# Kernel optimization log

Measured on AMD Instinct MI355X. Metric: run time of the kernel, lower is better.

The kernel has to match this reference:

```python
import jax, jax.numpy as jnp
import numpy as np

BN_EPS = 1e-5

def conv1x1(x, w, b):
    # x: (b, c, t, h, w); w: (o, c); b: (o,)
    return jnp.einsum('bcthw,oc->bothw', x, w) + b[None, :, None, None, None]

def pool_1x2x2(x):
    # MaxPool3d(kernel=(1,2,2), stride=(1,2,2))
    b, c, t, h, w = x.shape
    return x.reshape(b, c, t, h // 2, 2, w // 2, 2).max(axis=(4, 6))

def setup_inputs() -> dict:
    key = jax.random.key(0)
    ks = jax.random.split(key, 12)
    B, C, CI, T, H, W = 2, 256, 128, 16, 28, 28
    s_in = 1.0 / np.sqrt(C)
    s_ci = 1.0 / np.sqrt(CI)
    return {
        'x': jax.random.normal(ks[0], (B, C, T, H, W), jnp.float32),
        'mask_pred': jax.random.normal(ks[1], (B, C, T, H, W), jnp.float32),
        'g_w': jax.random.normal(ks[2], (CI, C), jnp.float32) * s_in,
        'g_b': jax.random.normal(ks[3], (CI,), jnp.float32) * s_in,
        'theta_w': jax.random.normal(ks[4], (CI, C), jnp.float32) * s_in,
        'theta_b': jax.random.normal(ks[5], (CI,), jnp.float32) * s_in,
        'phi_w': jax.random.normal(ks[6], (CI, C), jnp.float32) * s_in,
        'phi_b': jax.random.normal(ks[7], (CI,), jnp.float32) * s_in,
        'W_w': jax.random.normal(ks[8], (C, CI), jnp.float32) * s_ci,
        'W_b': jax.random.normal(ks[9], (C,), jnp.float32) * s_ci,
        'bn_gamma': jax.random.normal(ks[10], (C,), jnp.float32) * 0.1 + 1.0,
        'bn_beta': jax.random.normal(ks[11], (C,), jnp.float32) * 0.1,
    }

def reference(x, mask_pred, g_w, g_b, theta_w, theta_b, phi_w, phi_b, W_w, W_b, bn_gamma, bn_beta):
    B, C, T, H, W = x.shape
    CI = g_w.shape[0]
    # g and phi: 1x1 conv then (1,2,2) max-pool (sub_sample=True)
    g_x = pool_1x2x2(conv1x1(x, g_w, g_b)).reshape(B, CI, -1)          # (b, ci, Ns)
    g_x = g_x.transpose(0, 2, 1)                                        # (b, Ns, ci)
    theta = conv1x1(mask_pred, theta_w, theta_b).reshape(B, CI, -1)     # (b, ci, N)
    theta = theta.transpose(0, 2, 1)                                    # (b, N, ci)
    phi = pool_1x2x2(conv1x1(x, phi_w, phi_b)).reshape(B, CI, -1)       # (b, ci, Ns)
    f = jnp.einsum('bnc,bcm->bnm', theta, phi)                          # (b, N, Ns)
    f_div_C = jax.nn.softmax(f, axis=1)                                 # softmax over N (dim=1)
    y = jnp.einsum('bnm,bmc->bnc', f_div_C, g_x)                        # (b, N, ci)
    y = y.transpose(0, 2, 1).reshape(B, CI, T, H, W)
    W_y = conv1x1(y, W_w, W_b)                                          # (b, c, t, h, w)
    # BatchNorm3d in training mode (batch statistics over b,t,h,w)
    mean = W_y.mean(axis=(0, 2, 3, 4), keepdims=True)
    var = W_y.var(axis=(0, 2, 3, 4), keepdims=True)
    W_y = (W_y - mean) * jax.lax.rsqrt(var + BN_EPS)
    W_y = W_y * bn_gamma[None, :, None, None, None] + bn_beta[None, :, None, None, None]
    return W_y + x
```

## Files before the change

### kernel.cpp

```cpp
#include <hip/hip_runtime.h>


#define B_ 2
#define C_ 256
#define CI_ 128
#define NPIX 12544
#define NS 3136
#define NSL 28

typedef short bf16x8 __attribute__((ext_vector_type(8)));
typedef float f32x4 __attribute__((ext_vector_type(4)));

__device__ __forceinline__ short f2bf(float f) {
    unsigned u = __float_as_uint(f);
    u = (u + 0x7fff + ((u >> 16) & 1)) >> 16;
    return (short)u;
}
__device__ __forceinline__ float bf2f(short s) {
    return __uint_as_float(((unsigned)(unsigned short)s) << 16);
}
__device__ __forceinline__ short f2h(float f) {
    _Float16 h = (_Float16)f;
    short s;
    __builtin_memcpy(&s, &h, 2);
    return s;
}
__device__ __forceinline__ float h2f(short s) {
    _Float16 h;
    __builtin_memcpy(&h, &s, 2);
    return (float)h;
}
__device__ __forceinline__ f32x4 mfma16(bf16x8 a, bf16x8 b, f32x4 c) {
    return __builtin_amdgcn_mfma_f32_16x16x32_bf16(a, b, c, 0, 0, 0);
}
__device__ __forceinline__ size_t pidx(int r, int k) {
    return (size_t)((r >> 4) * 4 + (k >> 5)) * 512 +
           (size_t)(((k >> 3) & 3) * 128 + (r & 15) * 8 + (k & 7));
}
__device__ __forceinline__ size_t pidx256(int r, int k) {
    return (size_t)((r >> 4) * 8 + (k >> 5)) * 512 +
           (size_t)(((k >> 3) & 3) * 128 + (r & 15) * 8 + (k & 7));
}

struct Frag3 { bf16x8 h, m, l; };
struct Frag2 { bf16x8 h, m; };

__device__ __forceinline__ Frag3 ld3(const short* __restrict__ h, const short* __restrict__ m,
                                     const short* __restrict__ l, size_t off) {
    Frag3 f;
    f.h = *(const bf16x8*)(h + off);
    f.m = *(const bf16x8*)(m + off);
    f.l = *(const bf16x8*)(l + off);
    return f;
}
__device__ __forceinline__ Frag2 ld2(const short* __restrict__ h, const short* __restrict__ m,
                                     size_t off) {
    Frag2 f;
    f.h = *(const bf16x8*)(h + off);
    f.m = *(const bf16x8*)(m + off);
    return f;
}
__device__ __forceinline__ f32x4 mm5(Frag2 a, Frag3 w, f32x4 acc) {
    acc = mfma16(a.h, w.l, acc);
    acc = mfma16(a.m, w.m, acc);
    acc = mfma16(a.m, w.h, acc);
    acc = mfma16(a.h, w.m, acc);
    acc = mfma16(a.h, w.h, acc);
    return acc;
}
__device__ __forceinline__ f32x4 mm3(Frag2 a, Frag2 b, f32x4 acc) {
    acc = mfma16(a.m, b.h, acc);
    acc = mfma16(a.h, b.m, acc);
    acc = mfma16(a.h, b.h, acc);
    return acc;
}
__device__ __forceinline__ f32x4 mm2s(bf16x8 ah, Frag2 b, f32x4 acc) {
    acc = mfma16(ah, b.m, acc);
    acc = mfma16(ah, b.h, acc);
    return acc;
}
__device__ __forceinline__ bf16x8 mk_pa(f32x4 f0, f32x4 f1, int srcLo, int srcHi, bool hiTile) {
    unsigned t0d0 = (unsigned)(unsigned short)f2bf(__expf(f0[0] - 32.f)) |
                    ((unsigned)(unsigned short)f2bf(__expf(f0[1] - 32.f)) << 16);
    unsigned t0d1 = (unsigned)(unsigned short)f2bf(__expf(f0[2] - 32.f)) |
                    ((unsigned)(unsigned short)f2bf(__expf(f0[3] - 32.f)) << 16);
    unsigned t1d0 = (unsigned)(unsigned short)f2bf(__expf(f1[0] - 32.f)) |
                    ((unsigned)(unsigned short)f2bf(__expf(f1[1] - 32.f)) << 16);
    unsigned t1d1 = (unsigned)(unsigned short)f2bf(__expf(f1[2] - 32.f)) |
                    ((unsigned)(unsigned short)f2bf(__expf(f1[3] - 32.f)) << 16);
    unsigned lo0t0 = __shfl(t0d0, srcLo), lo1t0 = __shfl(t0d1, srcLo);
    unsigned hi0t0 = __shfl(t0d0, srcHi), hi1t0 = __shfl(t0d1, srcHi);
    unsigned lo0t1 = __shfl(t1d0, srcLo), lo1t1 = __shfl(t1d1, srcLo);
    unsigned hi0t1 = __shfl(t1d0, srcHi), hi1t1 = __shfl(t1d1, srcHi);
    unsigned pd[4];
    pd[0] = hiTile ? lo0t1 : lo0t0;
    pd[1] = hiTile ? lo1t1 : lo1t0;
    pd[2] = hiTile ? hi0t1 : hi0t0;
    pd[3] = hiTile ? hi1t1 : hi1t0;
    bf16x8 pa;
    __builtin_memcpy(&pa, pd, 16);
    return pa;
}

__global__ void k_splitw(const float* __restrict__ thw, const float* __restrict__ phw,
                         const float* __restrict__ gw, const float* __restrict__ Ww,
                         short* __restrict__ thwH, short* __restrict__ thwM, short* __restrict__ thwL,
                         short* __restrict__ phwH, short* __restrict__ phwM, short* __restrict__ phwL,
                         short* __restrict__ gwH, short* __restrict__ gwM,
                         short* __restrict__ wwH, short* __restrict__ wwM) {
    int i = blockIdx.x * 256 + threadIdx.x;
    int which = i >> 15, j = i & 32767;
    if (which == 0) {
        float x = thw[j];
        unsigned uh = __float_as_uint(x) & 0xffff0000u;
        float r1 = x - __uint_as_float(uh);
        unsigned um = __float_as_uint(r1) & 0xffff0000u;
        thwH[j] = (short)(uh >> 16);
        thwM[j] = (short)(um >> 16);
        thwL[j] = f2bf(r1 - __uint_as_float(um));
    } else if (which == 1) {
        float x = phw[j];
        unsigned uh = __float_as_uint(x) & 0xffff0000u;
        float r1 = x - __uint_as_float(uh);
        unsigned um = __float_as_uint(r1) & 0xffff0000u;
        phwH[j] = (short)(uh >> 16);
        phwM[j] = (short)(um >> 16);
        phwL[j] = f2bf(r1 - __uint_as_float(um));
    } else if (which == 2) {
        float x = gw[j];
        unsigned uh = __float_as_uint(x) & 0xffff0000u;
        gwH[j] = (short)(uh >> 16);
        gwM[j] = f2bf(x - __uint_as_float(uh));
    } else {
        float x = Ww[j];
        unsigned uh = __float_as_uint(x) & 0xffff0000u;
        wwH[j] = (short)(uh >> 16);
        wwM[j] = f2bf(x - __uint_as_float(uh));
    }
}

__global__ void k_transpose2p(const float* __restrict__ src, short* __restrict__ oh,
                              short* __restrict__ om) {
    __shared__ float tile[32][33];
    int b = blockIdx.z;
    const float* s = src + (size_t)b * C_ * NPIX;
    size_t ob = (size_t)b * NPIX * C_;
    int p0 = blockIdx.x * 32, c0 = blockIdx.y * 32;
    for (int i = threadIdx.y; i < 32; i += 8)
        tile[i][threadIdx.x] = s[(size_t)(c0 + i) * NPIX + p0 + threadIdx.x];
    __syncthreads();
    for (int i = threadIdx.y; i < 32; i += 8) {
        float v = tile[threadIdx.x][i];
        unsigned uh = __float_as_uint(v) & 0xffff0000u;
        size_t o = ob + pidx256(p0 + i, c0 + threadIdx.x);
        oh[o] = (short)(uh >> 16);
        om[o] = f2bf(v - __uint_as_float(uh));
    }
}

__global__ __launch_bounds__(128, 2) void k_conv5(const short* __restrict__ AH,
        const short* __restrict__ AM,
        const short* __restrict__ WH, const short* __restrict__ WM, const short* __restrict__ WL,
        const float* __restrict__ bias, short* __restrict__ oh, short* __restrict__ om) {
    int wid = threadIdx.x >> 6, lane = threadIdx.x & 63;
    int quad = lane >> 4, l16 = lane & 15;
    int b = blockIdx.y;
    size_t ab = (size_t)b * NPIX * C_;
    size_t ob = (size_t)b * NPIX * CI_;
    int rt0 = blockIdx.x * 2;
    f32x4 acc[2][4] = {};
    for (int kt = 0; kt < 8; kt++) {
        Frag2 a0 = ld2(AH, AM, ab + ((size_t)rt0 * 8 + kt) * 512 + lane * 8);
        Frag2 a1 = ld2(AH, AM, ab + ((size_t)(rt0 + 1) * 8 + kt) * 512 + lane * 8);
#pragma unroll
        for (int c4 = 0; c4 < 4; c4++) {
            int c = (wid * 4 + c4) * 16 + l16;
            Frag3 w = ld3(WH, WM, WL, (size_t)c * C_ + kt * 32 + quad * 8);
            acc[0][c4] = mm5(a0, w, acc[0][c4]);
            acc[1][c4] = mm5(a1, w, acc[1][c4]);
        }
    }
#pragma unroll
    for (int t2 = 0; t2 < 2; t2++)
#pragma unroll
        for (int c4 = 0; c4 < 4; c4++) {
            int c = (wid * 4 + c4) * 16 + l16;
            float bv = bias[c];
#pragma unroll
            for (int r = 0; r < 4; r++) {
                float v = acc[t2][c4][r] + bv;
                unsigned uh = __float_as_uint(v) & 0xffff0000u;
                size_t o = ob + pidx((rt0 + t2) * 16 + quad * 4 + r, c);
                oh[o] = (short)(uh >> 16);
                om[o] = f2bf(v - __uint_as_float(uh));
            }
        }
}

__global__ __launch_bounds__(128, 2) void k_convxg5(const short* __restrict__ AH,
        const short* __restrict__ AM,
        const short* __restrict__ PH, const short* __restrict__ PM, const short* __restrict__ PL,
        const short* __restrict__ GH, const short* __restrict__ GM,
        const float* __restrict__ pbias, const float* __restrict__ gbias,
        float* __restrict__ pfull, short* __restrict__ gout) {
    int wid = threadIdx.x >> 6, lane = threadIdx.x & 63;
    int quad = lane >> 4, l16 = lane & 15;
    int b = blockIdx.y;
    size_t ab = (size_t)b * NPIX * C_;
    float* Pb = pfull + (size_t)b * NPIX * CI_;
    short* Gb = gout + (size_t)b * NPIX * CI_;
    int rt0 = blockIdx.x * 2;
    f32x4 accp[2][4] = {}, accg[2][4] = {};
    for (int kt = 0; kt < 8; kt++) {
        Frag2 a0 = ld2(AH, AM, ab + ((size_t)rt0 * 8 + kt) * 512 + lane * 8);
        Frag2 a1 = ld2(AH, AM, ab + ((size_t)(rt0 + 1) * 8 + kt) * 512 + lane * 8);
#pragma unroll
        for (int c4 = 0; c4 < 4; c4++) {
            int c = (wid * 4 + c4) * 16 + l16;
            size_t wo = (size_t)c * C_ + kt * 32 + quad * 8;
            Frag3 wp = ld3(PH, PM, PL, wo);
            accp[0][c4] = mm5(a0, wp, accp[0][c4]);
            accp[1][c4] = mm5(a1, wp, accp[1][c4]);
            Frag2 wg = ld2(GH, GM, wo);
            accg[0][c4] = mm3(a0, wg, accg[0][c4]);
            accg[1][c4] = mm3(a1, wg, accg[1][c4]);
        }
    }
#pragma unroll
    for (int t2 = 0; t2 < 2; t2++)
#pragma unroll
        for (int c4 = 0; c4 < 4; c4++) {
            int c = (wid * 4 + c4) * 16 + l16;
            float pbv = pbias[c], gbv = gbias[c];
#pragma unroll
            for (int r = 0; r < 4; r++) {
                size_t o = (size_t)((rt0 + t2) * 16 + quad * 4 + r) * CI_ + c;
                Pb[o] = accp[t2][c4][r] + pbv;
                Gb[o] = f2bf(accg[t2][c4][r] + gbv);
            }
        }
}

__global__ void k_pool(const float* __restrict__ pfull, const short* __restrict__ gfull,
                       short* __restrict__ pth, short* __restrict__ ptm,
                       float* __restrict__ gcf) {
    int b = blockIdx.y;
    int idx = blockIdx.x * 256 + threadIdx.x;
    int ci = idx & 127, m = idx >> 7;
    int t = m / 196, r2i = m - t * 196;
    int h2 = r2i / 14, w2 = r2i - h2 * 14;
    size_t p = (size_t)t * 784 + (size_t)(2 * h2) * 28 + 2 * w2;
    size_t i0 = (size_t)b * NPIX * CI_ + p * CI_ + ci;
    float pv = fmaxf(fmaxf(pfull[i0], pfull[i0 + CI_]),
                     fmaxf(pfull[i0 + 28 * CI_], pfull[i0 + 29 * CI_]));
    unsigned uh = __float_as_uint(pv) & 0xffff0000u;
    size_t ob = (size_t)b * NS * CI_ + pidx(m, ci);
    pth[ob] = (short)(uh >> 16);
    ptm[ob] = f2bf(pv - __uint_as_float(uh));
    float g0 = fmaxf(fmaxf(bf2f(gfull[i0]), bf2f(gfull[i0 + CI_])),
                     fmaxf(bf2f(gfull[i0 + 28 * CI_]), bf2f(gfull[i0 + 29 * CI_])));
    gcf[(size_t)b * NS * CI_ + (size_t)ci * NS + m] = g0;
}

__global__ __launch_bounds__(128, 2) void k_stats(
        const short* __restrict__ thh, const short* __restrict__ thm,
        const short* __restrict__ phh, const short* __restrict__ phm,
        float* __restrict__ Spart) {
    (void)thm;
    int wid = threadIdx.x >> 6, lane = threadIdx.x & 63;
    int quad = lane >> 4, l16 = lane & 15;
    int wg = blockIdx.x;
    int p = wg % 56;
    int bx = wg / 56;
    int b = p & 1, ychunk = p >> 1;
    size_t tb = (size_t)b * NPIX * CI_, pb = (size_t)b * NS * CI_;
    int mtA = bx * 4 + wid * 2;
    Frag2 bfA[4], bfB[4];
#pragma unroll
    for (int kk = 0; kk < 4; kk++) {
        bfA[kk] = ld2(phh, phm, pb + ((size_t)mtA * 4 + kk) * 512 + lane * 8);
        bfB[kk] = ld2(phh, phm, pb + ((size_t)(mtA + 1) * 4 + kk) * 512 + lane * 8);
    }
    float SA = 0.f, SB = 0.f;
    int t_beg = ychunk * (784 / NSL), t_end = t_beg + 784 / NSL;
    for (int t = t_beg; t < t_end; t += 2) {
        f32x4 aA0 = {}, aA1 = {}, aB0 = {}, aB1 = {};
#pragma unroll
        for (int kk = 0; kk < 4; kk++) {
            bf16x8 x0 = *(const bf16x8*)(thh + tb + ((size_t)t * 4 + kk) * 512 + lane * 8);
            bf16x8 x1 = *(const bf16x8*)(thh + tb + ((size_t)(t + 1) * 4 + kk) * 512 + lane * 8);
            aA0 = mm2s(x0, bfA[kk], aA0);
            aA1 = mm2s(x1, bfA[kk], aA1);
            aB0 = mm2s(x0, bfB[kk], aB0);
            aB1 = mm2s(x1, bfB[kk], aB1);
        }
        SA += __expf(aA0[0] - 32.f) + __expf(aA0[1] - 32.f) +
              __expf(aA0[2] - 32.f) + __expf(aA0[3] - 32.f) +
              __expf(aA1[0] - 32.f) + __expf(aA1[1] - 32.f) +
              __expf(aA1[2] - 32.f) + __expf(aA1[3] - 32.f);
        SB += __expf(aB0[0] - 32.f) + __expf(aB0[1] - 32.f) +
              __expf(aB0[2] - 32.f) + __expf(aB0[3] - 32.f) +
              __expf(aB1[0] - 32.f) + __expf(aB1[1] - 32.f) +
              __expf(aB1[2] - 32.f) + __expf(aB1[3] - 32.f);
    }
    SA += __shfl_xor(SA, 16, 64); SA += __shfl_xor(SA, 32, 64);
    SB += __shfl_xor(SB, 16, 64); SB += __shfl_xor(SB, 32, 64);
    if (quad == 0) {
        size_t o = ((size_t)(b * NSL + ychunk)) * NS;
        Spart[o + mtA * 16 + l16] = SA;
        Spart[o + (mtA + 1) * 16 + l16] = SB;
    }
}

__global__ void k_combine(const float* __restrict__ Spart, float* __restrict__ wS) {
    int i = blockIdx.x * 256 + threadIdx.x;
    if (i >= B_ * NS) return;
    int b = i / NS, m = i - b * NS;
    float s = 0.f;
#pragma unroll
    for (int sl = 0; sl < NSL; sl++)
        s += Spart[((size_t)(b * NSL + sl)) * NS + m];
    wS[i] = 1.f / s;
}

__global__ void k_gscale(const float* __restrict__ gcf, const float* __restrict__ wS,
                         short* __restrict__ gc) {
    int i = blockIdx.x * 256 + threadIdx.x;
    int b = i / (CI_ * (NS / 8));
    int rem = i - b * CI_ * (NS / 8);
    int c = rem / (NS / 8);
    int m8 = rem - c * (NS / 8);
    int m = m8 * 8;
    const float* gr = gcf + ((size_t)b * CI_ + c) * NS + m;
    const float* wr = wS + (size_t)b * NS + m;
    short* go = gc + (size_t)b * NS * CI_ + ((size_t)(m8 >> 2) * 8 + (c >> 4)) * 512 +
                (m8 & 3) * 128 + (c & 15) * 8;
#pragma unroll
    for (int j = 0; j < 8; j++) go[j] = f2bf(gr[j] * wr[j]);
}

__global__ __launch_bounds__(128, 2) void k_pv(
        const short* __restrict__ thh, const short* __restrict__ thm,
        const short* __restrict__ phh, const short* __restrict__ phm,
        const short* __restrict__ gp, short* __restrict__ part) {
    int wid = threadIdx.x >> 6, lane = threadIdx.x & 63;
    int quad = lane >> 4, l16 = lane & 15;
    int wg = blockIdx.x;
    int pair = wg & 7;
    int bx = wg >> 3;
    int slice = pair >> 1, b = pair & 1;
    int ntA = bx * 4 + wid * 2;
    size_t tb = (size_t)b * NPIX * CI_, pb = (size_t)b * NS * CI_;
    const short* gpb = gp + (size_t)b * NS * CI_;
    Frag2 afA[4], afB[4];
#pragma unroll
    for (int kk = 0; kk < 4; kk++) {
        afA[kk] = ld2(thh, thm, tb + ((size_t)ntA * 4 + kk) * 512 + lane * 8);
        afB[kk] = ld2(thh, thm, tb + ((size_t)(ntA + 1) * 4 + kk) * 512 + lane * 8);
    }
    f32x4 yaccA[8] = {}, yaccB[8] = {};
    int srcLo = ((2 * quad) & 3) * 16 + l16;
    int srcHi = ((2 * quad + 1) & 3) * 16 + l16;
    bool hiTile = quad >= 2;
    int s_beg = slice * 24 + (slice < 2 ? slice : 2);
    int s_end = s_beg + 24 + (slice < 2 ? 1 : 0);
    for (int s = s_beg; s < s_end; s++) {
        bf16x8 gf0 = *(const bf16x8*)(gpb + (size_t)s * 4096 + 0 * 512 + lane * 8);
        bf16x8 gf1 = *(const bf16x8*)(gpb + (size_t)s * 4096 + 1 * 512 + lane * 8);
        bf16x8 gf2 = *(const bf16x8*)(gpb + (size_t)s * 4096 + 2 * 512 + lane * 8);
        bf16x8 gf3 = *(const bf16x8*)(gpb + (size_t)s * 4096 + 3 * 512 + lane * 8);
        bf16x8 gf4 = *(const bf16x8*)(gpb + (size_t)s * 4096 + 4 * 512 + lane * 8);
        bf16x8 gf5 = *(const bf16x8*)(gpb + (size_t)s * 4096 + 5 * 512 + lane * 8);
        bf16x8 gf6 = *(const bf16x8*)(gpb + (size_t)s * 4096 + 6 * 512 + lane * 8);
        bf16x8 gf7 = *(const bf16x8*)(gpb + (size_t)s * 4096 + 7 * 512 + lane * 8);
        f32x4 fA0 = {}, fA1 = {}, fB0 = {}, fB1 = {};
#pragma unroll
        for (int kk = 0; kk < 4; kk++) {
            Frag2 p0 = ld2(phh, phm, pb + ((size_t)(2 * s) * 4 + kk) * 512 + lane * 8);
            Frag2 p1 = ld2(phh, phm, pb + ((size_t)(2 * s + 1) * 4 + kk) * 512 + lane * 8);
            fA0 = mm3(p0, afA[kk], fA0);
            fA1 = mm3(p1, afA[kk], fA1);
            fB0 = mm3(p0, afB[kk], fB0);
            fB1 = mm3(p1, afB[kk], fB1);
        }
        bf16x8 paA = mk_pa(fA0, fA1, srcLo, srcHi, hiTile);
        bf16x8 paB = mk_pa(fB0, fB1, srcLo, srcHi, hiTile);
        yaccA[0] = mfma16(paA, gf0, yaccA[0]); yaccB[0] = mfma16(paB, gf0, yaccB[0]);
        yaccA[1] = mfma16(paA, gf1, yaccA[1]); yaccB[1] = mfma16(paB, gf1, yaccB[1]);
        yaccA[2] = mfma16(paA, gf2, yaccA[2]); yaccB[2] = mfma16(paB, gf2, yaccB[2]);
        yaccA[3] = mfma16(paA, gf3, yaccA[3]); yaccB[3] = mfma16(paB, gf3, yaccB[3]);
        yaccA[4] = mfma16(paA, gf4, yaccA[4]); yaccB[4] = mfma16(paB, gf4, yaccB[4]);
        yaccA[5] = mfma16(paA, gf5, yaccA[5]); yaccB[5] = mfma16(paB, gf5, yaccB[5]);
        yaccA[6] = mfma16(paA, gf6, yaccA[6]); yaccB[6] = mfma16(paB, gf6, yaccB[6]);
        yaccA[7] = mfma16(paA, gf7, yaccA[7]); yaccB[7] = mfma16(paB, gf7, yaccB[7]);
    }
    short* po = part + ((size_t)slice * B_ + b) * NPIX * CI_;
#pragma unroll
    for (int cc = 0; cc < 8; cc++)
#pragma unroll
        for (int r = 0; r < 4; r++) {
            po[pidx(ntA * 16 + quad * 4 + r, cc * 16 + l16)] = f2h(yaccA[cc][r]);
            po[pidx((ntA + 1) * 16 + quad * 4 + r, cc * 16 + l16)] = f2h(yaccB[cc][r]);
        }
}

__global__ void k_ycombine(const short* __restrict__ part, short* __restrict__ yh,
                           short* __restrict__ ym) {
    size_t i = (size_t)blockIdx.x * 256 + threadIdx.x;
    const size_t n = (size_t)B_ * NPIX * CI_;
    if (i >= n) return;
    float v = h2f(part[i]) + h2f(part[n + i]) + h2f(part[2 * n + i]) + h2f(part[3 * n + i]);
    unsigned uh = __float_as_uint(v) & 0xffff0000u;
    yh[i] = (short)(uh >> 16);
    ym[i] = f2bf(v - __uint_as_float(uh));
}

__global__ __launch_bounds__(256) void k_wconv3(const short* __restrict__ yh,
        const short* __restrict__ ym, const short* __restrict__ WH,
        const short* __restrict__ WM, const float* __restrict__ bias,
        float* __restrict__ Wy, float* __restrict__ stat) {
    int wid = threadIdx.x >> 6, lane = threadIdx.x & 63;
    int quad = lane >> 4, l16 = lane & 15;
    int b = blockIdx.z;
    size_t yb = (size_t)b * NPIX * CI_;
    float* Wyb = Wy + (size_t)b * NPIX * C_;
    int tile = blockIdx.x * 4 + wid;
    int row0 = tile * 16;
    int col0 = blockIdx.y * 128;
    f32x4 acc[8] = {};
#pragma unroll
    for (int kk = 0; kk < 4; kk++) {
        size_t ao = yb + ((size_t)tile * 4 + kk) * 512 + lane * 8;
        bf16x8 ah = *(const bf16x8*)(yh + ao);
        bf16x8 am = *(const bf16x8*)(ym + ao);
#pragma unroll
        for (int cc = 0; cc < 8; cc++) {
            Frag2 w = ld2(WH, WM, (size_t)(col0 + cc * 16 + l16) * CI_ + kk * 32 + quad * 8);
            acc[cc] = mfma16(am, w.h, acc[cc]);
            acc[cc] = mfma16(ah, w.m, acc[cc]);
            acc[cc] = mfma16(ah, w.h, acc[cc]);
        }
    }
#pragma unroll
    for (int cc = 0; cc < 8; cc++) {
        int c = col0 + cc * 16 + l16;
        float bv = bias[c];
        float s1 = 0.f, s2 = 0.f;
#pragma unroll
        for (int r = 0; r < 4; r++) {
            float v = acc[cc][r] + bv;
            Wyb[(size_t)(row0 + quad * 4 + r) * C_ + c] = v;
            s1 += v;
            s2 += v * v;
        }
        s1 += __shfl_xor(s1, 16, 64); s1 += __shfl_xor(s1, 32, 64);
        s2 += __shfl_xor(s2, 16, 64); s2 += __shfl_xor(s2, 32, 64);
        if (quad == 0) {
            atomicAdd(&stat[c], s1);
            atomicAdd(&stat[C_ + c], s2);
        }
    }
}

__global__ void k_bnfin(const float* __restrict__ stat, const float* __restrict__ gamma,
                        const float* __restrict__ beta, float* __restrict__ sc,
                        float* __restrict__ sh) {
    int c = threadIdx.x;
    const float inv = 1.f / (float)(B_ * NPIX);
    float mean = stat[c] * inv;
    float var = stat[C_ + c] * inv - mean * mean;
    float s = gamma[c] * rsqrtf(var + 1e-5f);
    sc[c] = s;
    sh[c] = beta[c] - mean * s;
}

__global__ void k_final(const float* __restrict__ Wy, const float* __restrict__ x,
                        const float* __restrict__ sc, const float* __restrict__ sh,
                        float* __restrict__ out) {
    __shared__ float tile[32][33];
    int b = blockIdx.z;
    const float* Wyb = Wy + (size_t)b * NPIX * C_;
    const float* xb = x + (size_t)b * C_ * NPIX;
    float* ob = out + (size_t)b * C_ * NPIX;
    int p0 = blockIdx.x * 32, c0 = blockIdx.y * 32;
    for (int i = threadIdx.y; i < 32; i += 8)
        tile[i][threadIdx.x] = Wyb[(size_t)(p0 + i) * C_ + c0 + threadIdx.x];
    __syncthreads();
    for (int i = threadIdx.y; i < 32; i += 8) {
        int c = c0 + i;
        size_t o = (size_t)c * NPIX + p0 + threadIdx.x;
        ob[o] = tile[threadIdx.x][i] * sc[c] + sh[c] + xb[o];
    }
}

extern "C" void kernel_launch(void* const* d_in, const int* in_sizes, int n_in,
                              void* d_out, int out_size, void* d_ws, size_t ws_size,
                              hipStream_t stream) {
    (void)in_sizes; (void)n_in; (void)out_size; (void)ws_size;
    const float* x     = (const float*)d_in[0];
    const float* mask  = (const float*)d_in[1];
    const float* g_w   = (const float*)d_in[2];
    const float* g_b   = (const float*)d_in[3];
    const float* th_w  = (const float*)d_in[4];
    const float* th_b  = (const float*)d_in[5];
    const float* ph_w  = (const float*)d_in[6];
    const float* ph_b  = (const float*)d_in[7];
    const float* W_w   = (const float*)d_in[8];
    const float* W_b   = (const float*)d_in[9];
    const float* gamma = (const float*)d_in[10];
    const float* beta  = (const float*)d_in[11];
    float* out = (float*)d_out;

    char* ws = (char*)d_ws;
    short* AH    = (short*)(ws + 0);
    short* AM    = (short*)(ws + 12845056);
    float* gcf   = (float*)(ws + 0);
    float* Spart = (float*)(ws + 4194304);
    float* wS    = (float*)(ws + 5242880);
    short* part  = (short*)(ws + 0);
    float* Wy    = (float*)(ws + 0);
    short* thH   = (short*)(ws + 25690112);
    short* thM   = (short*)(ws + 32112640);
    short* wwH   = (short*)(ws + 38535168);
    short* wwM   = wwH + 32768;
    float* pfull = (float*)(ws + 44957696);
    short* yH    = (short*)(ws + 44957696);
    short* yM    = (short*)(ws + 51380224);
    short* gfull = (short*)(ws + 57802752);
    short* thwH  = (short*)(ws + 64225280);
    short* thwM  = thwH + 32768;
    short* thwL  = thwM + 32768;
    short* phwH  = thwL + 32768;
    short* phwM  = phwH + 32768;
    short* phwL  = phwM + 32768;
    short* gwH   = phwL + 32768;
    short* gwM   = gwH + 32768;
    short* ptH   = (short*)(ws + 64225280);
    short* ptM   = (short*)(ws + 65830912);
    short* gc    = (short*)(ws + 69042176);
    float* stat  = (float*)(ws + 71099392);
    float* sc    = (float*)(ws + 71101440);
    float* sh    = (float*)(ws + 71102464);

    hipMemsetAsync(stat, 0, 2048, stream);

    k_splitw<<<512, 256, 0, stream>>>(th_w, ph_w, g_w, W_w, thwH, thwM, thwL,
                                      phwH, phwM, phwL, gwH, gwM, wwH, wwM);

    dim3 tb32(32, 8);
    k_transpose2p<<<dim3(NPIX / 32, C_ / 32, B_), tb32, 0, stream>>>(mask, AH, AM);
    k_conv5<<<dim3(NPIX / 32, B_), 128, 0, stream>>>(AH, AM, thwH, thwM, thwL, th_b, thH, thM);

    k_transpose2p<<<dim3(NPIX / 32, C_ / 32, B_), tb32, 0, stream>>>(x, AH, AM);
    k_convxg5<<<dim3(NPIX / 32, B_), 128, 0, stream>>>(AH, AM, phwH, phwM, phwL, gwH, gwM,
                                                       ph_b, g_b, pfull, gfull);

    k_pool<<<dim3(NS * CI_ / 256, B_), 256, 0, stream>>>(pfull, gfull, ptH, ptM, gcf);

    k_stats<<<49 * 56, 128, 0, stream>>>(thH, thM, ptH, ptM, Spart);
    k_combine<<<(B_ * NS + 255) / 256, 256, 0, stream>>>(Spart, wS);
    k_gscale<<<(B_ * CI_ * (NS / 8)) / 256, 256, 0, stream>>>(gcf, wS, gc);

    k_pv<<<196 * 8, 128, 0, stream>>>(thH, thM, ptH, ptM, gc, part);

    k_ycombine<<<(int)(((size_t)B_ * NPIX * CI_ + 255) / 256), 256, 0, stream>>>(part, yH, yM);

    k_wconv3<<<dim3(NPIX / 64, C_ / 128, B_), 256, 0, stream>>>(yH, yM, wwH, wwM, W_b, Wy, stat);
    k_bnfin<<<1, 256, 0, stream>>>(stat, gamma, beta, sc, sh);
    k_final<<<dim3(NPIX / 32, C_ / 32, B_), tb32, 0, stream>>>(Wy, x, sc, sh, out);
}
```

Measured before the change: 501.8 us.

## Materialize softmax exponentials in workspace instead of recomputing scores in PV pass

The stats kernel now also writes the exponentiated attention scores as a bf16 P matrix, laid out for MFMA fragments, into a large workspace buffer. A new PV kernel reads P directly and multiplies it by the scaled g values. This removes the second theta·phi score computation and exp from the PV pass. In exchange it writes and reads roughly 157 MB of P through memory, and it only runs when the workspace is large enough; otherwise the old path is used.

```diff
diff --git a/kernel.cpp b/kernel.cpp
--- a/kernel.cpp
+++ b/kernel.cpp
@@ -262,11 +262,64 @@
     gcf[(size_t)b * NS * CI_ + (size_t)ci * NS + m] = g0;
 }
 
+__global__ __launch_bounds__(128, 2) void k_statsP(
+        const short* __restrict__ thh, const short* __restrict__ phh,
+        const short* __restrict__ phm, float* __restrict__ Spart,
+        short* __restrict__ Pbuf) {
+    int wid = threadIdx.x >> 6, lane = threadIdx.x & 63;
+    int quad = lane >> 4, l16 = lane & 15;
+    int wg = blockIdx.x;
+    int p = wg % 56;
+    int bx = wg / 56;
+    int b = p & 1, ychunk = p >> 1;
+    size_t tb = (size_t)b * NPIX * CI_, pb = (size_t)b * NS * CI_;
+    short* PB = Pbuf + (size_t)b * NPIX * NS;
+    int mtA = bx * 4 + wid * 2;
+    Frag2 bfA[4], bfB[4];
+#pragma unroll
+    for (int kk = 0; kk < 4; kk++) {
+        bfA[kk] = ld2(phh, phm, pb + ((size_t)mtA * 4 + kk) * 512 + lane * 8);
+        bfB[kk] = ld2(phh, phm, pb + ((size_t)(mtA + 1) * 4 + kk) * 512 + lane * 8);
+    }
+    float SA = 0.f, SB = 0.f;
+    int t_beg = ychunk * (784 / NSL), t_end = t_beg + 784 / NSL;
+    int kg = mtA >> 1;
+    size_t laneoff = (size_t)(l16 >> 3) * 128 + (l16 & 7) + (size_t)quad * 32;
+    for (int t = t_beg; t < t_end; t += 2) {
+        f32x4 aA0 = {}, aA1 = {}, aB0 = {}, aB1 = {};
+#pragma unroll
+        for (int kk = 0; kk < 4; kk++) {
+            bf16x8 x0 = *(const bf16x8*)(thh + tb + ((size_t)t * 4 + kk) * 512 + lane * 8);
+            bf16x8 x1 = *(const bf16x8*)(thh + tb + ((size_t)(t + 1) * 4 + kk) * 512 + lane * 8);
+            aA0 = mm2s(x0, bfA[kk], aA0);
+            aA1 = mm2s(x1, bfA[kk], aA1);
+            aB0 = mm2s(x0, bfB[kk], aB0);
+            aB1 = mm2s(x1, bfB[kk], aB1);
+        }
+        size_t cA0 = ((size_t)t * 98 + kg) * 512 + laneoff;
+        size_t cA1 = cA0 + 98 * 512;
+        size_t cB0 = cA0 + 256;
+        size_t cB1 = cA1 + 256;
+#pragma unroll
+        for (int r = 0; r < 4; r++) {
+            float eA0 = __expf(aA0[r] - 32.f); SA += eA0; PB[cA0 + r * 8] = f2bf(eA0);
+            float eA1 = __expf(aA1[r] - 32.f); SA += eA1; PB[cA1 + r * 8] = f2bf(eA1);
+            float eB0 = __expf(aB0[r] - 32.f); SB += eB0; PB[cB0 + r * 8] = f2bf(eB0);
+            float eB1 = __expf(aB1[r] - 32.f); SB += eB1; PB[cB1 + r * 8] = f2bf(eB1);
+        }
+    }
+    SA += __shfl_xor(SA, 16, 64); SA += __shfl_xor(SA, 32, 64);
+    SB += __shfl_xor(SB, 16, 64); SB += __shfl_xor(SB, 32, 64);
+    if (quad == 0) {
+        size_t o = ((size_t)(b * NSL + ychunk)) * NS;
+        Spart[o + mtA * 16 + l16] = SA;
+        Spart[o + (mtA + 1) * 16 + l16] = SB;
+    }
+}
+
 __global__ __launch_bounds__(128, 2) void k_stats(
-        const short* __restrict__ thh, const short* __restrict__ thm,
-        const short* __restrict__ phh, const short* __restrict__ phm,
-        float* __restrict__ Spart) {
-    (void)thm;
+        const short* __restrict__ thh, const short* __restrict__ phh,
+        const short* __restrict__ phm, float* __restrict__ Spart) {
     int wid = threadIdx.x >> 6, lane = threadIdx.x & 63;
     int quad = lane >> 4, l16 = lane & 15;
     int wg = blockIdx.x;
@@ -337,6 +390,56 @@
                 (m8 & 3) * 128 + (c & 15) * 8;
 #pragma unroll
     for (int j = 0; j < 8; j++) go[j] = f2bf(gr[j] * wr[j]);
+}
+
+__global__ __launch_bounds__(128, 2) void k_pvP(
+        const short* __restrict__ Pbuf, const short* __restrict__ gp,
+        short* __restrict__ part) {
+    int wid = threadIdx.x >> 6, lane = threadIdx.x & 63;
+    int quad = lane >> 4, l16 = lane & 15;
+    int wg = blockIdx.x;
+    int pair = wg & 7;
+    int bx = wg >> 3;
+    int slice = pair >> 1, b = pair & 1;
+    int ntA = bx * 4 + wid * 2;
+    const short* PB = Pbuf + (size_t)b * NPIX * NS;
+    const short* gpb = gp + (size_t)b * NS * CI_;
+    f32x4 yaccA[8] = {}, yaccB[8] = {};
+    int s_beg = slice * 24 + (slice < 2 ? slice : 2);
+    int s_end = s_beg + 24 + (slice < 2 ? 1 : 0);
+    const short* pA = PB + ((size_t)ntA * 98 + s_beg) * 512 + lane * 8;
+    const short* pBp = PB + ((size_t)(ntA + 1) * 98 + s_beg) * 512 + lane * 8;
+    const short* gb = gpb + (size_t)s_beg * 4096 + lane * 8;
+#pragma unroll 2
+    for (int s = s_beg; s < s_end; s++) {
+        bf16x8 pa0 = *(const bf16x8*)pA;
+        bf16x8 pa1 = *(const bf16x8*)pBp;
+        bf16x8 g0 = *(const bf16x8*)(gb + 0 * 512);
+        bf16x8 g1 = *(const bf16x8*)(gb + 1 * 512);
+        bf16x8 g2 = *(const bf16x8*)(gb + 2 * 512);
+        bf16x8 g3 = *(const bf16x8*)(gb + 3 * 512);
+        bf16x8 g4 = *(const bf16x8*)(gb + 4 * 512);
+        bf16x8 g5 = *(const bf16x8*)(gb + 5 * 512);
+        bf16x8 g6 = *(const bf16x8*)(gb + 6 * 512);
+        bf16x8 g7 = *(const bf16x8*)(gb + 7 * 512);
+        pA += 512; pBp += 512; gb += 4096;
+        yaccA[0] = mfma16(pa0, g0, yaccA[0]); yaccB[0] = mfma16(pa1, g0, yaccB[0]);
+        yaccA[1] = mfma16(pa0, g1, yaccA[1]); yaccB[1] = mfma16(pa1, g1, yaccB[1]);
+        yaccA[2] = mfma16(pa0, g2, yaccA[2]); yaccB[2] = mfma16(pa1, g2, yaccB[2]);
+        yaccA[3] = mfma16(pa0, g3, yaccA[3]); yaccB[3] = mfma16(pa1, g3, yaccB[3]);
+        yaccA[4] = mfma16(pa0, g4, yaccA[4]); yaccB[4] = mfma16(pa1, g4, yaccB[4]);
+        yaccA[5] = mfma16(pa0, g5, yaccA[5]); yaccB[5] = mfma16(pa1, g5, yaccB[5]);
+        yaccA[6] = mfma16(pa0, g6, yaccA[6]); yaccB[6] = mfma16(pa1, g6, yaccB[6]);
+        yaccA[7] = mfma16(pa0, g7, yaccA[7]); yaccB[7] = mfma16(pa1, g7, yaccB[7]);
+    }
+    short* po = part + ((size_t)slice * B_ + b) * NPIX * CI_;
+#pragma unroll
+    for (int cc = 0; cc < 8; cc++)
+#pragma unroll
+        for (int r = 0; r < 4; r++) {
+            po[pidx(ntA * 16 + quad * 4 + r, cc * 16 + l16)] = f2h(yaccA[cc][r]);
+            po[pidx((ntA + 1) * 16 + quad * 4 + r, cc * 16 + l16)] = f2h(yaccB[cc][r]);
+        }
 }
 
 __global__ __launch_bounds__(128, 2) void k_pv(
@@ -496,7 +599,7 @@
 extern "C" void kernel_launch(void* const* d_in, const int* in_sizes, int n_in,
                               void* d_out, int out_size, void* d_ws, size_t ws_size,
                               hipStream_t stream) {
-    (void)in_sizes; (void)n_in; (void)out_size; (void)ws_size;
+    (void)in_sizes; (void)n_in; (void)out_size;
     const float* x     = (const float*)d_in[0];
     const float* mask  = (const float*)d_in[1];
     const float* g_w   = (const float*)d_in[2];
@@ -541,6 +644,10 @@
     float* stat  = (float*)(ws + 71099392);
     float* sc    = (float*)(ws + 71101440);
     float* sh    = (float*)(ws + 71102464);
+    const size_t pOff = 71303168ull;
+    const size_t pBytes = (size_t)B_ * NPIX * NS * sizeof(short);
+    bool bigws = ws_size >= pOff + pBytes;
+    short* Pbuf = (short*)(ws + pOff);
 
     hipMemsetAsync(stat, 0, 2048, stream);
 
@@ -557,11 +664,17 @@
 
     k_pool<<<dim3(NS * CI_ / 256, B_), 256, 0, stream>>>(pfull, gfull, ptH, ptM, gcf);
 
-    k_stats<<<49 * 56, 128, 0, stream>>>(thH, thM, ptH, ptM, Spart);
+    if (bigws)
+        k_statsP<<<49 * 56, 128, 0, stream>>>(thH, ptH, ptM, Spart, Pbuf);
+    else
+        k_stats<<<49 * 56, 128, 0, stream>>>(thH, ptH, ptM, Spart);
     k_combine<<<(B_ * NS + 255) / 256, 256, 0, stream>>>(Spart, wS);
     k_gscale<<<(B_ * CI_ * (NS / 8)) / 256, 256, 0, stream>>>(gcf, wS, gc);
 
-    k_pv<<<196 * 8, 128, 0, stream>>>(thH, thM, ptH, ptM, gc, part);
+    if (bigws)
+        k_pvP<<<196 * 8, 128, 0, stream>>>(Pbuf, gc, part);
+    else
+        k_pv<<<196 * 8, 128, 0, stream>>>(thH, thM, ptH, ptM, gc, part);
 
     k_ycombine<<<(int)(((size_t)B_ * NPIX * CI_ + 255) / 256), 256, 0, stream>>>(part, yH, yM);
 
```

Measured after the change: 447.0 us. 10.9% less time.
